# Optimization experiments

Measured on AMD Instinct MI355X. Metric: run time of the kernel, lower is better.

The kernel has to match this reference:

```python
import jax, jax.numpy as jnp
import numpy as np

D = 64
V_ITEM, V_GENRE, V_USER = 100001, 21, 1000001
B, L, G = 16384, 200, 6
LAM = 0.001  # time_decay_lambda


def _ln(x, g, b):
    m = jnp.mean(x, axis=-1, keepdims=True)
    v = jnp.var(x, axis=-1, keepdims=True)
    return (x - m) / jnp.sqrt(v + 1e-5) * g + b


def _mlp(x, w1, b1, g, be, w2, b2):
    h = jax.nn.relu(_ln(x @ w1.T + b1, g, be))
    return h @ w2.T + b2


def _l2norm(x):
    return x / jnp.maximum(jnp.linalg.norm(x, axis=1, keepdims=True), 1e-12)


def _wmean(emb, w):  # emb [B,S,D], w [B,S,1]
    return (emb * w).sum(axis=1) / (w.sum(axis=1) + 1e-8)


def setup_inputs() -> dict:
    key = jax.random.key(0)
    ks = jax.random.split(key, 32)
    n = lambda k, s: (0.02 * jax.random.normal(k, s)).astype(jnp.float32)
    emb_item = n(ks[0], (V_ITEM, D)).at[0].set(0.0)
    emb_genre = n(ks[1], (V_GENRE, D)).at[0].set(0.0)
    emb_user = n(ks[2], (V_USER, D)).at[0].set(0.0)
    inp = {
        'user_id': jax.random.randint(ks[3], (B,), 0, V_USER),
        'history': jax.random.randint(ks[4], (B, L), 0, V_ITEM),
        'top_genres': jax.random.randint(ks[5], (B, G), 0, V_GENRE),
        'item_id': jax.random.randint(ks[6], (B,), 0, V_ITEM),
        'tmdb_genres': jax.random.randint(ks[7], (B, G), 0, V_GENRE),
        'history_ts_diff': jax.random.uniform(ks[8], (B, L)) * 1000.0,
        'u_avg_rating': jax.random.normal(ks[9], (B,)),
        'activity': jax.random.normal(ks[10], (B,)),
        'release_year': jax.random.normal(ks[11], (B,)),
        'i_avg_rating': jax.random.normal(ks[12], (B,)),
        'revenue': jax.random.normal(ks[13], (B,)),
        'emb_item': emb_item, 'emb_genre': emb_genre, 'emb_user': emb_user,
        # user tower params
        'ut_cont_w': n(ks[14], (D, 2)), 'ut_cont_b': n(ks[15], (D,)),
        'ut_w1': n(ks[16], (2 * D, 4 * D)), 'ut_b1': n(ks[17], (2 * D,)),
        'ut_g': jnp.ones((2 * D,), jnp.float32), 'ut_be': jnp.zeros((2 * D,), jnp.float32),
        'ut_w2': n(ks[18], (D, 2 * D)), 'ut_b2': n(ks[19], (D,)),
        # item tower params
        'it_cont_w': n(ks[20], (D, 3)), 'it_cont_b': n(ks[21], (D,)),
        'it_w1': n(ks[22], (2 * D, 3 * D)), 'it_b1': n(ks[23], (2 * D,)),
        'it_g': jnp.ones((2 * D,), jnp.float32), 'it_be': jnp.zeros((2 * D,), jnp.float32),
        'it_w2': n(ks[24], (D, 2 * D)), 'it_b2': n(ks[25], (D,)),
    }
    return inp


def reference(user_id, history, top_genres, item_id, tmdb_genres,
              history_ts_diff, u_avg_rating, activity, release_year, i_avg_rating, revenue,
              emb_item, emb_genre, emb_user,
              ut_cont_w, ut_cont_b, ut_w1, ut_b1, ut_g, ut_be, ut_w2, ut_b2,
              it_cont_w, it_cont_b, it_w1, it_b1, it_g, it_be, it_w2, it_b2):
    # ----- user tower -----
    u_e = emb_user[user_id]                                   # [B,D]
    hist_e = emb_item[history]                                # [B,L,D]
    hist_mask = (history > 0).astype(jnp.float32)             # [B,L]
    tw = jnp.exp(-LAM * history_ts_diff)                      # time decay
    cw = (tw * hist_mask)[..., None]                          # [B,L,1]
    hist_pool = _wmean(hist_e, cw)                            # [B,D]
    ug_e = emb_genre[top_genres]                              # [B,G,D]
    ug_mask = (top_genres > 0).astype(jnp.float32)[..., None]
    ug_pool = _wmean(ug_e, ug_mask)
    u_cont = jax.nn.relu(jnp.stack([u_avg_rating, activity], axis=1) @ ut_cont_w.T + ut_cont_b)
    u_cat = jnp.concatenate([u_e, hist_pool, ug_pool, u_cont], axis=1)  # [B,4D]
    u_out = _l2norm(_mlp(u_cat, ut_w1, ut_b1, ut_g, ut_be, ut_w2, ut_b2))
    # ----- item tower -----
    i_e = emb_item[item_id]
    ig_e = emb_genre[tmdb_genres]
    ig_mask = (tmdb_genres > 0).astype(jnp.float32)[..., None]
    ig_pool = _wmean(ig_e, ig_mask)
    i_cont = jax.nn.relu(jnp.stack([release_year, i_avg_rating, revenue], axis=1) @ it_cont_w.T + it_cont_b)
    i_cat = jnp.concatenate([i_e, ig_pool, i_cont], axis=1)   # [B,3D]
    i_out = _l2norm(_mlp(i_cat, it_w1, it_b1, it_g, it_be, it_w2, it_b2))
    return (u_out, i_out)
```

## Files before the change

kernel.cpp:

```cpp
#include <hip/hip_runtime.h>

#define DD 64
#define LL 200
#define GG 6
#define LAMBDA 0.001f
#define PREP_BLOCKS 3126

#if __has_builtin(__builtin_amdgcn_cvt_scalef32_pk_f32_fp4) && __has_builtin(__builtin_amdgcn_cvt_scalef32_pk_fp4_f32)
#define USE_FP4 1
#else
#define USE_FP4 0
#endif

typedef __attribute__((ext_vector_type(8))) short s8v;
typedef __attribute__((ext_vector_type(4))) float f4v;
typedef __attribute__((ext_vector_type(2))) float f2v;

__device__ __forceinline__ float wave_reduce_sum(float v) {
    #pragma unroll
    for (int off = 32; off > 0; off >>= 1)
        v += __shfl_xor(v, off, 64);
    return v;
}

__device__ __forceinline__ unsigned short f2bf(float f) {
    union { float f; unsigned int u; } v; v.f = f;
    return (unsigned short)((v.u + 0x7FFFu + ((v.u >> 16) & 1u)) >> 16);
}

__global__ __launch_bounds__(256)
void prep_kernel(const float* __restrict__ emb_item,
                 const float* __restrict__ ut_w1, const float* __restrict__ ut_w2,
                 const float* __restrict__ it_w1, const float* __restrict__ it_w2,
                 unsigned int* __restrict__ emb_tab,
                 unsigned short* __restrict__ blob, int V)
{
    if (blockIdx.x < PREP_BLOCKS) {
        const int i = blockIdx.x * 256 + threadIdx.x;
#if USE_FP4
        if (i < V * 8) {
            const int v = i >> 3, c = i & 7;
            const float4 f0 = *(const float4*)&emb_item[(size_t)v * 64 + c * 8];
            const float4 f1 = *(const float4*)&emb_item[(size_t)v * 64 + c * 8 + 4];
            unsigned int o = 0;
            o = __builtin_amdgcn_cvt_scalef32_pk_fp4_f32(o, f0.x * 64.f, f0.y * 64.f, 1.0f, 0);
            o = __builtin_amdgcn_cvt_scalef32_pk_fp4_f32(o, f0.z * 64.f, f0.w * 64.f, 1.0f, 1);
            o = __builtin_amdgcn_cvt_scalef32_pk_fp4_f32(o, f1.x * 64.f, f1.y * 64.f, 1.0f, 2);
            o = __builtin_amdgcn_cvt_scalef32_pk_fp4_f32(o, f1.z * 64.f, f1.w * 64.f, 1.0f, 3);
            emb_tab[i] = o;
        }
#else
        if (i < V * 8) {
            const float4 f0 = *(const float4*)&emb_item[(size_t)i * 8];
            const float4 f1 = *(const float4*)&emb_item[(size_t)i * 8 + 4];
            int lo = __builtin_amdgcn_cvt_pk_fp8_f32(f0.x * 64.f, f0.y * 64.f, 0, false);
            lo     = __builtin_amdgcn_cvt_pk_fp8_f32(f0.z * 64.f, f0.w * 64.f, lo, true);
            int hi = __builtin_amdgcn_cvt_pk_fp8_f32(f1.x * 64.f, f1.y * 64.f, 0, false);
            hi     = __builtin_amdgcn_cvt_pk_fp8_f32(f1.z * 64.f, f1.w * 64.f, hi, true);
            uint2 o; o.x = (unsigned int)lo; o.y = (unsigned int)hi;
            *(uint2*)&emb_tab[(size_t)i * 2] = o;
        }
#endif
        return;
    }
    const int s = (blockIdx.x - PREP_BLOCKS) * 256 + threadIdx.x;
    if (s >= 9216) return;
    const float* src; int K, NT, r, k8; size_t obase;
    if (s < 4096)      { src = ut_w1; K = 256; NT = 8; r = s >> 5;          k8 = s & 31;          obase = 0; }
    else if (s < 5120) { src = ut_w2; K = 128; NT = 4; r = (s-4096) >> 4;   k8 = (s-4096) & 15;   obase = 4096; }
    else if (s < 8192) { src = it_w1; K = 192; NT = 8; r = (s-5120) / 24;   k8 = (s-5120) % 24;   obase = 5120; }
    else               { src = it_w2; K = 128; NT = 4; r = (s-8192) >> 4;   k8 = (s-8192) & 15;   obase = 8192; }
    const int k = k8 * 8;
    const float4 f0 = *(const float4*)&src[(size_t)r * K + k];
    const float4 f1 = *(const float4*)&src[(size_t)r * K + k + 4];
    const int ks = k >> 5, lg = (k >> 3) & 3;
    const int lp = lg * 16 + (r & 15), nt = r >> 4;
    const size_t slot = obase + (size_t)(ks * NT + nt) * 64 + lp;
    s8v wv;
    wv[0]=(short)f2bf(f0.x); wv[1]=(short)f2bf(f0.y); wv[2]=(short)f2bf(f0.z); wv[3]=(short)f2bf(f0.w);
    wv[4]=(short)f2bf(f1.x); wv[5]=(short)f2bf(f1.y); wv[6]=(short)f2bf(f1.z); wv[7]=(short)f2bf(f1.w);
    *(s8v*)&blob[slot * 8] = wv;
}

__global__ __launch_bounds__(256)
void hist_pool_kernel(const int* __restrict__ history,
                      const float* __restrict__ ts_diff,
                      const unsigned int* __restrict__ emb_tab,
                      float* __restrict__ hist_out, int B)
{
    const int wave = threadIdx.x >> 6;
    const int lane = threadIdx.x & 63;
    const int b = blockIdx.x * 4 + wave;
    const int grp = lane >> 3;
    const int c8 = lane & 7;

    __shared__ float2 s_p[4][LL];

    const int*   hrow = history + (size_t)b * LL;
    const float* trow = ts_diff + (size_t)b * LL;

    float wpart = 0.f;
    #pragma unroll
    for (int l = lane; l < LL; l += 64) {
        int idx = 0; float w = 0.f;
        const int raw = hrow[l];
        if (raw > 0) { w = __expf(-LAMBDA * trow[l]); idx = raw; }
        s_p[wave][l] = make_float2(w, __int_as_float(idx));
        wpart += w;
    }
    const float wsum = wave_reduce_sum(wpart);
    __syncthreads();

    float a[8];
    #pragma unroll
    for (int j = 0; j < 8; ++j) a[j] = 0.f;

#if USE_FP4
    #define GATHER_DECODE(EW, N, BASE)                                           \
        do {                                                                     \
            unsigned int e_[N]; float w_[N];                                     \
            _Pragma("unroll")                                                    \
            for (int i = 0; i < N; ++i) {                                        \
                const float2 p = s_p[wave][(BASE) + i * 8 + grp];                \
                w_[i] = p.x;                                                     \
                e_[i] = emb_tab[(size_t)__float_as_int(p.y) * 8 + c8];           \
            }                                                                    \
            _Pragma("unroll")                                                    \
            for (int i = 0; i < N; ++i) {                                        \
                const f2v d01 = __builtin_amdgcn_cvt_scalef32_pk_f32_fp4(e_[i], 1.0f, 0); \
                const f2v d23 = __builtin_amdgcn_cvt_scalef32_pk_f32_fp4(e_[i], 1.0f, 1); \
                const f2v d45 = __builtin_amdgcn_cvt_scalef32_pk_f32_fp4(e_[i], 1.0f, 2); \
                const f2v d67 = __builtin_amdgcn_cvt_scalef32_pk_f32_fp4(e_[i], 1.0f, 3); \
                a[0] = fmaf(w_[i], d01[0], a[0]);                                \
                a[1] = fmaf(w_[i], d01[1], a[1]);                                \
                a[2] = fmaf(w_[i], d23[0], a[2]);                                \
                a[3] = fmaf(w_[i], d23[1], a[3]);                                \
                a[4] = fmaf(w_[i], d45[0], a[4]);                                \
                a[5] = fmaf(w_[i], d45[1], a[5]);                                \
                a[6] = fmaf(w_[i], d67[0], a[6]);                                \
                a[7] = fmaf(w_[i], d67[1], a[7]);                                \
            }                                                                    \
        } while (0)
#else
    #define GATHER_DECODE(EW, N, BASE)                                           \
        do {                                                                     \
            uint2 e_[N]; float w_[N];                                            \
            _Pragma("unroll")                                                    \
            for (int i = 0; i < N; ++i) {                                        \
                const float2 p = s_p[wave][(BASE) + i * 8 + grp];                \
                w_[i] = p.x;                                                     \
                e_[i] = *(const uint2*)&emb_tab[(size_t)__float_as_int(p.y) * 16 + c8 * 2]; \
            }                                                                    \
            _Pragma("unroll")                                                    \
            for (int i = 0; i < N; ++i) {                                        \
                const f2v d01 = __builtin_amdgcn_cvt_pk_f32_fp8((int)e_[i].x, false); \
                const f2v d23 = __builtin_amdgcn_cvt_pk_f32_fp8((int)e_[i].x, true);  \
                const f2v d45 = __builtin_amdgcn_cvt_pk_f32_fp8((int)e_[i].y, false); \
                const f2v d67 = __builtin_amdgcn_cvt_pk_f32_fp8((int)e_[i].y, true);  \
                a[0] = fmaf(w_[i], d01[0], a[0]);                                \
                a[1] = fmaf(w_[i], d01[1], a[1]);                                \
                a[2] = fmaf(w_[i], d23[0], a[2]);                                \
                a[3] = fmaf(w_[i], d23[1], a[3]);                                \
                a[4] = fmaf(w_[i], d45[0], a[4]);                                \
                a[5] = fmaf(w_[i], d45[1], a[5]);                                \
                a[6] = fmaf(w_[i], d67[0], a[6]);                                \
                a[7] = fmaf(w_[i], d67[1], a[7]);                                \
            }                                                                    \
        } while (0)
#endif

    GATHER_DECODE(unsigned int, 16, 0);
    GATHER_DECODE(unsigned int, 9, 128);

    #pragma unroll
    for (int off = 8; off <= 32; off <<= 1)
        #pragma unroll
        for (int j = 0; j < 8; ++j)
            a[j] += __shfl_xor(a[j], off, 64);

    if (grp == 0) {
        const float inv = 0.015625f / (wsum + 1e-8f);
        float4 o0 = make_float4(a[0]*inv, a[1]*inv, a[2]*inv, a[3]*inv);
        float4 o1 = make_float4(a[4]*inv, a[5]*inv, a[6]*inv, a[7]*inv);
        *(float4*)&hist_out[(size_t)b * DD + c8 * 8]     = o0;
        *(float4*)&hist_out[(size_t)b * DD + c8 * 8 + 4] = o1;
    }
}

#define PUT_FRAG(buf, NKS, r, d, val)                                   \
    do {                                                                \
        const int _mt = (r) >> 4, _ks = (d) >> 5;                       \
        const int _lp = (((d) >> 3) & 3) * 16 + ((r) & 15);             \
        (buf)[(((_mt) * (NKS) + _ks) * 64 + _lp) * 8 + ((d) & 7)] = f2bf(val); \
    } while (0)

__global__ __launch_bounds__(512)
void towers_kernel(
    const int* __restrict__ user_id, const int* __restrict__ top_genres,
    const int* __restrict__ item_id, const int* __restrict__ tmdb_genres,
    const float* __restrict__ hist_pool,
    const float* __restrict__ u_avg, const float* __restrict__ activity,
    const float* __restrict__ rel_year, const float* __restrict__ i_avg,
    const float* __restrict__ revenue,
    const float* __restrict__ emb_item, const float* __restrict__ emb_genre,
    const float* __restrict__ emb_user,
    const float* __restrict__ ut_cont_w, const float* __restrict__ ut_cont_b,
    const float* __restrict__ it_cont_w, const float* __restrict__ it_cont_b,
    const unsigned short* __restrict__ wblob,
    const float* __restrict__ ut_b1, const float* __restrict__ ut_g,
    const float* __restrict__ ut_be, const float* __restrict__ ut_b2,
    const float* __restrict__ it_b1, const float* __restrict__ it_g,
    const float* __restrict__ it_be, const float* __restrict__ it_b2,
    float* __restrict__ out, int B)
{
    const int tid = threadIdx.x, wave = tid >> 6, lane = tid & 63;
    const int nU = B / 16;
    const bool is_user = (int)blockIdx.x < nU;
    const int r0 = (is_user ? blockIdx.x : blockIdx.x - nU) * 16;

    __shared__ __align__(16) unsigned char  sXY[8 * 1024];
    __shared__ __align__(16) unsigned short sHf[4 * 64 * 8];
    __shared__ __align__(16) float sO[16 * 64];

    unsigned short* sXf = (unsigned short*)sXY;
    float* sY = (float*)sXY;

    const f4v zero4 = {0.f, 0.f, 0.f, 0.f};

    if (is_user) {
        #pragma unroll
        for (int i = 0; i < 2; ++i) {
            const int r = wave * 2 + i, b = r0 + r;
            const float ue = emb_user[(size_t)user_id[b] * DD + lane];
            const float hp = hist_pool[(size_t)b * DD + lane];
            const int* grow = top_genres + (size_t)b * GG;
            float gacc = 0.f, gw = 0.f;
            #pragma unroll
            for (int g = 0; g < GG; ++g) {
                const int idx = grow[g];
                const float m = (idx > 0) ? 1.f : 0.f;
                gacc = fmaf(m, emb_genre[idx * DD + lane], gacc);
                gw += m;
            }
            const float ug = gacc / (gw + 1e-8f);
            float uc = fmaf(u_avg[b], ut_cont_w[lane * 2 + 0],
                       fmaf(activity[b], ut_cont_w[lane * 2 + 1], ut_cont_b[lane]));
            uc = fmaxf(uc, 0.f);
            PUT_FRAG(sXf, 8, r, lane, ue);
            PUT_FRAG(sXf, 8, r, 64 + lane, hp);
            PUT_FRAG(sXf, 8, r, 128 + lane, ug);
            PUT_FRAG(sXf, 8, r, 192 + lane, uc);
        }
        __syncthreads();

        f4v acc = zero4;
        #pragma unroll
        for (int ks = 0; ks < 8; ++ks) {
            const s8v av = *(const s8v*)&sXf[(ks * 64 + lane) * 8];
            const s8v bv = *(const s8v*)&wblob[((ks * 8 + wave) * 64 + lane) * 8];
            acc = __builtin_amdgcn_mfma_f32_16x16x32_bf16(av, bv, acc, 0, 0, 0);
        }
        __syncthreads();

        {
            const int n = wave * 16 + (lane & 15);
            const float bb = ut_b1[n];
            #pragma unroll
            for (int rg = 0; rg < 4; ++rg) {
                const int m = (lane >> 4) * 4 + rg;
                sY[m * 128 + n] = acc[rg] + bb;
            }
        }
        __syncthreads();

        {
            const float g0 = ut_g[lane], g1 = ut_g[lane + 64];
            const float e0 = ut_be[lane], e1 = ut_be[lane + 64];
            #pragma unroll
            for (int i = 0; i < 2; ++i) {
                const int r = wave * 2 + i;
                const float a = sY[r * 128 + lane];
                const float c = sY[r * 128 + 64 + lane];
                const float mean = wave_reduce_sum(a + c) * (1.f / 128.f);
                const float da = a - mean, dc = c - mean;
                const float var = wave_reduce_sum(da * da + dc * dc) * (1.f / 128.f);
                const float rstd = rsqrtf(var + 1e-5f);
                const float h0 = fmaxf(fmaf(da * rstd, g0, e0), 0.f);
                const float h1 = fmaxf(fmaf(dc * rstd, g1, e1), 0.f);
                PUT_FRAG(sHf, 4, r, lane, h0);
                PUT_FRAG(sHf, 4, r, 64 + lane, h1);
            }
        }
        __syncthreads();

        if (wave < 4) {
            f4v acc2 = zero4;
            #pragma unroll
            for (int ks = 0; ks < 4; ++ks) {
                const s8v av = *(const s8v*)&sHf[(ks * 64 + lane) * 8];
                const s8v bv = *(const s8v*)&wblob[(4096 + (ks * 4 + wave) * 64 + lane) * 8];
                acc2 = __builtin_amdgcn_mfma_f32_16x16x32_bf16(av, bv, acc2, 0, 0, 0);
            }
            const int n = wave * 16 + (lane & 15);
            const float bb = ut_b2[n];
            #pragma unroll
            for (int rg = 0; rg < 4; ++rg) {
                const int m = (lane >> 4) * 4 + rg;
                sO[m * 64 + n] = acc2[rg] + bb;
            }
        }
        __syncthreads();

        #pragma unroll
        for (int i = 0; i < 2; ++i) {
            const int r = wave * 2 + i;
            const float o = sO[r * 64 + lane];
            const float nrm = sqrtf(wave_reduce_sum(o * o));
            out[(size_t)(r0 + r) * DD + lane] = o / fmaxf(nrm, 1e-12f);
        }
    } else {
        #pragma unroll
        for (int i = 0; i < 2; ++i) {
            const int r = wave * 2 + i, b = r0 + r;
            const float ie = emb_item[(size_t)item_id[b] * DD + lane];
            const int* grow = tmdb_genres + (size_t)b * GG;
            float gacc = 0.f, gw = 0.f;
            #pragma unroll
            for (int g = 0; g < GG; ++g) {
                const int idx = grow[g];
                const float m = (idx > 0) ? 1.f : 0.f;
                gacc = fmaf(m, emb_genre[idx * DD + lane], gacc);
                gw += m;
            }
            const float ig = gacc / (gw + 1e-8f);
            float ic = fmaf(rel_year[b], it_cont_w[lane * 3 + 0],
                       fmaf(i_avg[b],   it_cont_w[lane * 3 + 1],
                       fmaf(revenue[b], it_cont_w[lane * 3 + 2], it_cont_b[lane])));
            ic = fmaxf(ic, 0.f);
            PUT_FRAG(sXf, 6, r, lane, ie);
            PUT_FRAG(sXf, 6, r, 64 + lane, ig);
            PUT_FRAG(sXf, 6, r, 128 + lane, ic);
        }
        __syncthreads();

        f4v acc = zero4;
        #pragma unroll
        for (int ks = 0; ks < 6; ++ks) {
            const s8v av = *(const s8v*)&sXf[(ks * 64 + lane) * 8];
            const s8v bv = *(const s8v*)&wblob[(5120 + (ks * 8 + wave) * 64 + lane) * 8];
            acc = __builtin_amdgcn_mfma_f32_16x16x32_bf16(av, bv, acc, 0, 0, 0);
        }
        __syncthreads();

        {
            const int n = wave * 16 + (lane & 15);
            const float bb = it_b1[n];
            #pragma unroll
            for (int rg = 0; rg < 4; ++rg) {
                const int m = (lane >> 4) * 4 + rg;
                sY[m * 128 + n] = acc[rg] + bb;
            }
        }
        __syncthreads();

        {
            const float g0 = it_g[lane], g1 = it_g[lane + 64];
            const float e0 = it_be[lane], e1 = it_be[lane + 64];
            #pragma unroll
            for (int i = 0; i < 2; ++i) {
                const int r = wave * 2 + i;
                const float a = sY[r * 128 + lane];
                const float c = sY[r * 128 + 64 + lane];
                const float mean = wave_reduce_sum(a + c) * (1.f / 128.f);
                const float da = a - mean, dc = c - mean;
                const float var = wave_reduce_sum(da * da + dc * dc) * (1.f / 128.f);
                const float rstd = rsqrtf(var + 1e-5f);
                const float h0 = fmaxf(fmaf(da * rstd, g0, e0), 0.f);
                const float h1 = fmaxf(fmaf(dc * rstd, g1, e1), 0.f);
                PUT_FRAG(sHf, 4, r, lane, h0);
                PUT_FRAG(sHf, 4, r, 64 + lane, h1);
            }
        }
        __syncthreads();

        if (wave < 4) {
            f4v acc2 = zero4;
            #pragma unroll
            for (int ks = 0; ks < 4; ++ks) {
                const s8v av = *(const s8v*)&sHf[(ks * 64 + lane) * 8];
                const s8v bv = *(const s8v*)&wblob[(8192 + (ks * 4 + wave) * 64 + lane) * 8];
                acc2 = __builtin_amdgcn_mfma_f32_16x16x32_bf16(av, bv, acc2, 0, 0, 0);
            }
            const int n = wave * 16 + (lane & 15);
            const float bb = it_b2[n];
            #pragma unroll
            for (int rg = 0; rg < 4; ++rg) {
                const int m = (lane >> 4) * 4 + rg;
                sO[m * 64 + n] = acc2[rg] + bb;
            }
        }
        __syncthreads();

        #pragma unroll
        for (int i = 0; i < 2; ++i) {
            const int r = wave * 2 + i;
            const float o = sO[r * 64 + lane];
            const float nrm = sqrtf(wave_reduce_sum(o * o));
            out[(size_t)B * DD + (size_t)(r0 + r) * DD + lane] = o / fmaxf(nrm, 1e-12f);
        }
    }
}

extern "C" void kernel_launch(void* const* d_in, const int* in_sizes, int n_in,
                              void* d_out, int out_size, void* d_ws, size_t ws_size,
                              hipStream_t stream) {
    const int*   user_id     = (const int*)  d_in[0];
    const int*   history     = (const int*)  d_in[1];
    const int*   top_genres  = (const int*)  d_in[2];
    const int*   item_id     = (const int*)  d_in[3];
    const int*   tmdb_genres = (const int*)  d_in[4];
    const float* ts_diff     = (const float*)d_in[5];
    const float* u_avg       = (const float*)d_in[6];
    const float* activity    = (const float*)d_in[7];
    const float* rel_year    = (const float*)d_in[8];
    const float* i_avg       = (const float*)d_in[9];
    const float* revenue     = (const float*)d_in[10];
    const float* emb_item    = (const float*)d_in[11];
    const float* emb_genre   = (const float*)d_in[12];
    const float* emb_user    = (const float*)d_in[13];
    const float* ut_cont_w   = (const float*)d_in[14];
    const float* ut_cont_b   = (const float*)d_in[15];
    const float* ut_w1       = (const float*)d_in[16];
    const float* ut_b1       = (const float*)d_in[17];
    const float* ut_g        = (const float*)d_in[18];
    const float* ut_be       = (const float*)d_in[19];
    const float* ut_w2       = (const float*)d_in[20];
    const float* ut_b2       = (const float*)d_in[21];
    const float* it_cont_w   = (const float*)d_in[22];
    const float* it_cont_b   = (const float*)d_in[23];
    const float* it_w1       = (const float*)d_in[24];
    const float* it_b1       = (const float*)d_in[25];
    const float* it_g        = (const float*)d_in[26];
    const float* it_be       = (const float*)d_in[27];
    const float* it_w2       = (const float*)d_in[28];
    const float* it_b2       = (const float*)d_in[29];

    const int B = in_sizes[0];
    const int n_item = in_sizes[11];
    const int V = n_item / DD;

    unsigned int* emb_tab = (unsigned int*)d_ws;
    size_t off = (size_t)(n_item / 4) * sizeof(unsigned int);
    off = (off + 255) & ~(size_t)255;
    unsigned short* wblob = (unsigned short*)((char*)d_ws + off);
    off += (size_t)9216 * 8 * sizeof(unsigned short);
    off = (off + 255) & ~(size_t)255;
    float* hist_pool = (float*)((char*)d_ws + off);

    hipLaunchKernelGGL(prep_kernel, dim3(PREP_BLOCKS + 36), dim3(256), 0, stream,
        emb_item, ut_w1, ut_w2, it_w1, it_w2, emb_tab, wblob, V);

    hipLaunchKernelGGL(hist_pool_kernel, dim3(B / 4), dim3(256), 0, stream,
        history, ts_diff, emb_tab, hist_pool, B);

    hipLaunchKernelGGL(towers_kernel, dim3(2 * (B / 16)), dim3(512), 0, stream,
        user_id, top_genres, item_id, tmdb_genres, hist_pool,
        u_avg, activity, rel_year, i_avg, revenue,
        emb_item, emb_genre, emb_user,
        ut_cont_w, ut_cont_b, it_cont_w, it_cont_b,
        wblob, ut_b1, ut_g, ut_be, ut_b2, it_b1, it_g, it_be, it_b2,
        (float*)d_out, B);
}
```

Measured before the change: 51.49 us.

## Process 32 rows per towers block and drop redundant hist-pool barrier

The towers kernel now handles 32 batch rows per block instead of 16. Each weight fragment loaded for the first MLP GEMM is reused across two M-tiles, and all eight waves take part in the second GEMM instead of four. This halves the grid, cuts redundant weight fetches and idle waves, but doubles LDS use per block and may lower occupancy. Separately, the __syncthreads in hist_pool_kernel is removed because each wave only reads back its own shared-memory row.

After: 50.88 us. No clear change (-1.2%).

```diff
diff --git a/kernel.cpp b/kernel.cpp
--- a/kernel.cpp
+++ b/kernel.cpp
@@ -109,14 +109,13 @@
         wpart += w;
     }
     const float wsum = wave_reduce_sum(wpart);
-    __syncthreads();
 
     float a[8];
     #pragma unroll
     for (int j = 0; j < 8; ++j) a[j] = 0.f;
 
 #if USE_FP4
-    #define GATHER_DECODE(EW, N, BASE)                                           \
+    #define GATHER_DECODE(N, BASE)                                               \
         do {                                                                     \
             unsigned int e_[N]; float w_[N];                                     \
             _Pragma("unroll")                                                    \
@@ -142,7 +141,7 @@
             }                                                                    \
         } while (0)
 #else
-    #define GATHER_DECODE(EW, N, BASE)                                           \
+    #define GATHER_DECODE(N, BASE)                                               \
         do {                                                                     \
             uint2 e_[N]; float w_[N];                                            \
             _Pragma("unroll")                                                    \
@@ -169,8 +168,8 @@
         } while (0)
 #endif
 
-    GATHER_DECODE(unsigned int, 16, 0);
-    GATHER_DECODE(unsigned int, 9, 128);
+    GATHER_DECODE(16, 0);
+    GATHER_DECODE(9, 128);
 
     #pragma unroll
     for (int off = 8; off <= 32; off <<= 1)
@@ -214,23 +213,24 @@
     float* __restrict__ out, int B)
 {
     const int tid = threadIdx.x, wave = tid >> 6, lane = tid & 63;
-    const int nU = B / 16;
+    const int nU = B / 32;
     const bool is_user = (int)blockIdx.x < nU;
-    const int r0 = (is_user ? blockIdx.x : blockIdx.x - nU) * 16;
-
-    __shared__ __align__(16) unsigned char  sXY[8 * 1024];
-    __shared__ __align__(16) unsigned short sHf[4 * 64 * 8];
-    __shared__ __align__(16) float sO[16 * 64];
+    const int r0 = (is_user ? blockIdx.x : blockIdx.x - nU) * 32;
+
+    __shared__ __align__(16) unsigned char  sXY[16 * 1024];
+    __shared__ __align__(16) unsigned short sHf[2 * 4 * 64 * 8];
+    __shared__ __align__(16) float sO[32 * 64];
 
     unsigned short* sXf = (unsigned short*)sXY;
     float* sY = (float*)sXY;
 
     const f4v zero4 = {0.f, 0.f, 0.f, 0.f};
+    const int mh2 = wave >> 2, nh2 = wave & 3;
 
     if (is_user) {
         #pragma unroll
-        for (int i = 0; i < 2; ++i) {
-            const int r = wave * 2 + i, b = r0 + r;
+        for (int i = 0; i < 4; ++i) {
+            const int r = wave * 4 + i, b = r0 + r;
             const float ue = emb_user[(size_t)user_id[b] * DD + lane];
             const float hp = hist_pool[(size_t)b * DD + lane];
             const int* grow = top_genres + (size_t)b * GG;
@@ -253,12 +253,16 @@
         }
         __syncthreads();
 
-        f4v acc = zero4;
+        f4v acc[2];
+        acc[0] = zero4; acc[1] = zero4;
         #pragma unroll
         for (int ks = 0; ks < 8; ++ks) {
-            const s8v av = *(const s8v*)&sXf[(ks * 64 + lane) * 8];
             const s8v bv = *(const s8v*)&wblob[((ks * 8 + wave) * 64 + lane) * 8];
-            acc = __builtin_amdgcn_mfma_f32_16x16x32_bf16(av, bv, acc, 0, 0, 0);
+            #pragma unroll
+            for (int ml = 0; ml < 2; ++ml) {
+                const s8v av = *(const s8v*)&sXf[(((ml * 8 + ks)) * 64 + lane) * 8];
+                acc[ml] = __builtin_amdgcn_mfma_f32_16x16x32_bf16(av, bv, acc[ml], 0, 0, 0);
+            }
         }
         __syncthreads();
 
@@ -266,62 +270,69 @@
             const int n = wave * 16 + (lane & 15);
             const float bb = ut_b1[n];
             #pragma unroll
-            for (int rg = 0; rg < 4; ++rg) {
-                const int m = (lane >> 4) * 4 + rg;
-                sY[m * 128 + n] = acc[rg] + bb;
-            }
-        }
-        __syncthreads();
-
+            for (int ml = 0; ml < 2; ++ml)
+                #pragma unroll
+                for (int rg = 0; rg < 4; ++rg) {
+                    const int m = ml * 16 + (lane >> 4) * 4 + rg;
+                    sY[m * 128 + n] = acc[ml][rg] + bb;
+                }
+        }
+        __syncthreads();
+
+        float h0[4], h1[4];
         {
             const float g0 = ut_g[lane], g1 = ut_g[lane + 64];
             const float e0 = ut_be[lane], e1 = ut_be[lane + 64];
             #pragma unroll
-            for (int i = 0; i < 2; ++i) {
-                const int r = wave * 2 + i;
+            for (int i = 0; i < 4; ++i) {
+                const int r = wave * 4 + i;
                 const float a = sY[r * 128 + lane];
                 const float c = sY[r * 128 + 64 + lane];
                 const float mean = wave_reduce_sum(a + c) * (1.f / 128.f);
                 const float da = a - mean, dc = c - mean;
                 const float var = wave_reduce_sum(da * da + dc * dc) * (1.f / 128.f);
                 const float rstd = rsqrtf(var + 1e-5f);
-                const float h0 = fmaxf(fmaf(da * rstd, g0, e0), 0.f);
-                const float h1 = fmaxf(fmaf(dc * rstd, g1, e1), 0.f);
-                PUT_FRAG(sHf, 4, r, lane, h0);
-                PUT_FRAG(sHf, 4, r, 64 + lane, h1);
-            }
-        }
-        __syncthreads();
-
-        if (wave < 4) {
+                h0[i] = fmaxf(fmaf(da * rstd, g0, e0), 0.f);
+                h1[i] = fmaxf(fmaf(dc * rstd, g1, e1), 0.f);
+            }
+        }
+        #pragma unroll
+        for (int i = 0; i < 4; ++i) {
+            const int r = wave * 4 + i;
+            PUT_FRAG(sHf, 4, r, lane, h0[i]);
+            PUT_FRAG(sHf, 4, r, 64 + lane, h1[i]);
+        }
+        __syncthreads();
+
+        {
             f4v acc2 = zero4;
             #pragma unroll
             for (int ks = 0; ks < 4; ++ks) {
-                const s8v av = *(const s8v*)&sHf[(ks * 64 + lane) * 8];
-                const s8v bv = *(const s8v*)&wblob[(4096 + (ks * 4 + wave) * 64 + lane) * 8];
+                const s8v av = *(const s8v*)&sHf[((mh2 * 4 + ks) * 64 + lane) * 8];
+                const s8v bv = *(const s8v*)&wblob[(4096 + (ks * 4 + nh2) * 64 + lane) * 8];
                 acc2 = __builtin_amdgcn_mfma_f32_16x16x32_bf16(av, bv, acc2, 0, 0, 0);
             }
-            const int n = wave * 16 + (lane & 15);
+            const int n = nh2 * 16 + (lane & 15);
             const float bb = ut_b2[n];
             #pragma unroll
             for (int rg = 0; rg < 4; ++rg) {
-                const int m = (lane >> 4) * 4 + rg;
+                const int m = mh2 * 16 + (lane >> 4) * 4 + rg;
                 sO[m * 64 + n] = acc2[rg] + bb;
             }
         }
         __syncthreads();
 
         #pragma unroll
-        for (int i = 0; i < 2; ++i) {
-            const int r = wave * 2 + i;
+        for (int i = 0; i < 4; ++i) {
+            const int r = wave * 4 + i;
             const float o = sO[r * 64 + lane];
             const float nrm = sqrtf(wave_reduce_sum(o * o));
             out[(size_t)(r0 + r) * DD + lane] = o / fmaxf(nrm, 1e-12f);
         }
     } else {
         #pragma unroll
-        for (int i = 0; i < 2; ++i) {
-            const int r = wave * 2 + i, b = r0 + r;
+        for (int i = 0; i < 4; ++i) {
+            const int r = wave * 4 + i, b = r0 + r;
             const float ie = emb_item[(size_t)item_id[b] * DD + lane];
             const int* grow = tmdb_genres + (size_t)b * GG;
             float gacc = 0.f, gw = 0.f;
@@ -343,12 +354,16 @@
         }
         __syncthreads();
 
-        f4v acc = zero4;
+        f4v acc[2];
+        acc[0] = zero4; acc[1] = zero4;
         #pragma unroll
         for (int ks = 0; ks < 6; ++ks) {
-            const s8v av = *(const s8v*)&sXf[(ks * 64 + lane) * 8];
             const s8v bv = *(const s8v*)&wblob[(5120 + (ks * 8 + wave) * 64 + lane) * 8];
-            acc = __builtin_amdgcn_mfma_f32_16x16x32_bf16(av, bv, acc, 0, 0, 0);
+            #pragma unroll
+            for (int ml = 0; ml < 2; ++ml) {
+                const s8v av = *(const s8v*)&sXf[(((ml * 6 + ks)) * 64 + lane) * 8];
+                acc[ml] = __builtin_amdgcn_mfma_f32_16x16x32_bf16(av, bv, acc[ml], 0, 0, 0);
+            }
         }
         __syncthreads();
 
@@ -356,54 +371,61 @@
             const int n = wave * 16 + (lane & 15);
             const float bb = it_b1[n];
             #pragma unroll
-            for (int rg = 0; rg < 4; ++rg) {
-                const int m = (lane >> 4) * 4 + rg;
-                sY[m * 128 + n] = acc[rg] + bb;
-            }
-        }
-        __syncthreads();
-
+            for (int ml = 0; ml < 2; ++ml)
+                #pragma unroll
+                for (int rg = 0; rg < 4; ++rg) {
+                    const int m = ml * 16 + (lane >> 4) * 4 + rg;
+                    sY[m * 128 + n] = acc[ml][rg] + bb;
+                }
+        }
+        __syncthreads();
+
+        float h0[4], h1[4];
         {
             const float g0 = it_g[lane], g1 = it_g[lane + 64];
             const float e0 = it_be[lane], e1 = it_be[lane + 64];
             #pragma unroll
-            for (int i = 0; i < 2; ++i) {
-                const int r = wave * 2 + i;
+            for (int i = 0; i < 4; ++i) {
+                const int r = wave * 4 + i;
                 const float a = sY[r * 128 + lane];
                 const float c = sY[r * 128 + 64 + lane];
                 const float mean = wave_reduce_sum(a + c) * (1.f / 128.f);
                 const float da = a - mean, dc = c - mean;
                 const float var = wave_reduce_sum(da * da + dc * dc) * (1.f / 128.f);
                 const float rstd = rsqrtf(var + 1e-5f);
-                const float h0 = fmaxf(fmaf(da * rstd, g0, e0), 0.f);
-                const float h1 = fmaxf(fmaf(dc * rstd, g1, e1), 0.f);
-                PUT_FRAG(sHf, 4, r, lane, h0);
-                PUT_FRAG(sHf, 4, r, 64 + lane, h1);
-            }
-        }
-        __syncthreads();
-
-        if (wave < 4) {
+                h0[i] = fmaxf(fmaf(da * rstd, g0, e0), 0.f);
+                h1[i] = fmaxf(fmaf(dc * rstd, g1, e1), 0.f);
+            }
+        }
+        #pragma unroll
+        for (int i = 0; i < 4; ++i) {
+            const int r = wave * 4 + i;
+            PUT_FRAG(sHf, 4, r, lane, h0[i]);
+            PUT_FRAG(sHf, 4, r, 64 + lane, h1[i]);
+        }
+        __syncthreads();
+
+        {
             f4v acc2 = zero4;
             #pragma unroll
             for (int ks = 0; ks < 4; ++ks) {
-                const s8v av = *(const s8v*)&sHf[(ks * 64 + lane) * 8];
-                const s8v bv = *(const s8v*)&wblob[(8192 + (ks * 4 + wave) * 64 + lane) * 8];
+                const s8v av = *(const s8v*)&sHf[((mh2 * 4 + ks) * 64 + lane) * 8];
+                const s8v bv = *(const s8v*)&wblob[(8192 + (ks * 4 + nh2) * 64 + lane) * 8];
                 acc2 = __builtin_amdgcn_mfma_f32_16x16x32_bf16(av, bv, acc2, 0, 0, 0);
             }
-            const int n = wave * 16 + (lane & 15);
+            const int n = nh2 * 16 + (lane & 15);
             const float bb = it_b2[n];
             #pragma unroll
             for (int rg = 0; rg < 4; ++rg) {
-                const int m = (lane >> 4) * 4 + rg;
+                const int m = mh2 * 16 + (lane >> 4) * 4 + rg;
                 sO[m * 64 + n] = acc2[rg] + bb;
             }
         }
         __syncthreads();
 
         #pragma unroll
-        for (int i = 0; i < 2; ++i) {
-            const int r = wave * 2 + i;
+        for (int i = 0; i < 4; ++i) {
+            const int r = wave * 4 + i;
             const float o = sO[r * 64 + lane];
             const float nrm = sqrtf(wave_reduce_sum(o * o));
             out[(size_t)B * DD + (size_t)(r0 + r) * DD + lane] = o / fmaxf(nrm, 1e-12f);
@@ -463,7 +485,7 @@
     hipLaunchKernelGGL(hist_pool_kernel, dim3(B / 4), dim3(256), 0, stream,
         history, ts_diff, emb_tab, hist_pool, B);
 
-    hipLaunchKernelGGL(towers_kernel, dim3(2 * (B / 16)), dim3(512), 0, stream,
+    hipLaunchKernelGGL(towers_kernel, dim3(2 * (B / 32)), dim3(512), 0, stream,
         user_id, top_genres, item_id, tmdb_genres, hist_pool,
         u_avg, activity, rel_year, i_avg, revenue,
         emb_item, emb_genre, emb_user,
```
